# Performance work log

Measured on AMD Instinct MI355X. Metric: run time of the kernel, lower is better.

## Reference

```python
import jax, jax.numpy as jnp
import numpy as np


def _unpack_int4(packed):
    """Unpack bytes (stored as int32 in [0,256)) into signed int4 values in [-8,7].
    packed: [..., K/2] -> [..., K], low nibble first."""
    lo = packed & 0xF
    hi = (packed >> 4) & 0xF
    lo = lo - 16 * (lo >= 8).astype(jnp.int32)
    hi = hi - 16 * (hi >= 8).astype(jnp.int32)
    out = jnp.stack([lo, hi], axis=-1)
    return out.reshape(packed.shape[:-1] + (packed.shape[-1] * 2,))


def setup_inputs() -> dict:
    key = jax.random.key(0)
    ks = jax.random.split(key, 7)
    M, K, N, R = 8192, 4096, 4096, 32
    return {
        "x_quant": jax.random.randint(ks[0], (M, K // 2), 0, 256, dtype=jnp.int32),
        "x_scale": jax.random.uniform(ks[1], (M,), dtype=jnp.float32) * 0.01 + 1e-3,
        "weight": jax.random.randint(ks[2], (N, K // 2), 0, 256, dtype=jnp.int32),
        "weight_scales": jax.random.uniform(ks[3], (N,), dtype=jnp.float32) * 0.01 + 1e-3,
        "bias": jax.random.normal(ks[4], (N,), dtype=jnp.float32) * 0.01,
        "x_r": jax.random.normal(ks[5], (M, R), dtype=jnp.float32),
        "w_outlier": jax.random.normal(ks[6], (N, R), dtype=jnp.float32),
    }


def reference(x_quant, x_scale, weight, weight_scales, bias, x_r, w_outlier):
    # Unpack packed int4 operands: [M,K] and [N,K], values in [-8,7]
    xq = _unpack_int4(x_quant)
    wq = _unpack_int4(weight)
    # Integer GEMM (s4s4 accumulate in int32), then fused dequant + bias
    acc = jnp.matmul(xq, wq.T)  # [M, N] int32
    out = acc.astype(jnp.float32) * x_scale[:, None] * weight_scales[None, :] + bias[None, :]
    # Low-rank outlier correction: addmm_(x_r, w_outlier.T)
    out = out + jnp.matmul(x_r, w_outlier.T)
    return out
```

## Files before the change

kernel.cpp:

```cpp
#include <hip/hip_runtime.h>

#define M_ 8192
#define K_ 4096
#define N_ 4096
#define R_ 32
#define KP_ (K_ / 2)

#define BK 128
#define NKT 32
#define CHUNK 16384
#define GRID ((M_ / 128) * (N_ / 128))

typedef __attribute__((ext_vector_type(4)))  int    i32x4;
typedef __attribute__((ext_vector_type(16))) int    i32x16;
typedef __attribute__((ext_vector_type(4)))  float  f32x4;
typedef __attribute__((ext_vector_type(16))) float  f32x16;
typedef __attribute__((ext_vector_type(8)))  __bf16 bf16x8;

__device__ __forceinline__ void gload16(const void* g, void* l) {
  __builtin_amdgcn_global_load_lds(
      (const __attribute__((address_space(1))) unsigned int*)g,
      (__attribute__((address_space(3))) unsigned int*)l, 16, 0, 0);
}

__device__ __forceinline__ unsigned nib2(int b) {
  unsigned lo = (unsigned)(((b & 15) ^ 8) - 8) & 0xFFu;
  unsigned hi = (unsigned)((((b >> 4) & 15) ^ 8) - 8) & 0xFFu;
  return lo | (hi << 8);
}

__global__ void repack_tiles(const int* __restrict__ in, uint4* __restrict__ out) {
  int i = blockIdx.x * 256 + threadIdx.x;
  int l = i & 63;
  int u = (i >> 6) & 15;
  int tile = i >> 10;
  int row = (tile >> 6) * 256 + (u >> 1) * 32 + (l & 31);
  int w0  = (tile & 63) * 32 + (u & 1) * 16 + (l >> 5) * 8;
  const int4* p = (const int4*)(in + (size_t)row * KP_ + w0);
  int4 a = p[0], b = p[1];
  uint4 o;
  o.x = nib2(a.x) | (nib2(a.y) << 16);
  o.y = nib2(a.z) | (nib2(a.w) << 16);
  o.z = nib2(b.x) | (nib2(b.y) << 16);
  o.w = nib2(b.z) | (nib2(b.w) << 16);
  out[i] = o;
}

__device__ __forceinline__ unsigned short f2b(float x) {
  unsigned u = __float_as_uint(x);
  return (unsigned short)((u + 0x7FFFu + ((u >> 16) & 1u)) >> 16);
}

__global__ void f2bf4(const float* __restrict__ in, unsigned short* __restrict__ out, int n4) {
  int stride = gridDim.x * blockDim.x;
  for (int i = blockIdx.x * blockDim.x + threadIdx.x; i < n4; i += stride) {
    float4 f = ((const float4*)in)[i];
    ushort4 o;
    o.x = f2b(f.x); o.y = f2b(f.y); o.z = f2b(f.z); o.w = f2b(f.w);
    ((ushort4*)out)[i] = o;
  }
}

__global__ __launch_bounds__(256, 3) void gemm_w4a4(
    const char* __restrict__ x8t, const char* __restrict__ w8t,
    const unsigned short* __restrict__ xrb, const unsigned short* __restrict__ wob,
    const float* __restrict__ xscale, const float* __restrict__ wscale,
    const float* __restrict__ bias, float* __restrict__ out)
{
  __shared__ __align__(16) char lds[32768];

  const int t  = threadIdx.x;
  const int w  = t >> 6;
  const int l  = t & 63;
  const int lr = l & 31;
  const int lh = l >> 5;
  const int wr = w >> 1;
  const int wc = w & 1;

  const int xcd = blockIdx.x & 7;
  const int c   = blockIdx.x >> 3;
  const int mt  = (xcd & 3) * 16 + (c & 15);
  const int nt  = (xcd >> 2) * 16 + (c >> 4);
  const int m0  = mt * 128, n0 = nt * 128;

  const char* aT = x8t + (size_t)(mt >> 1) * 64 * CHUNK;
  const char* bT = w8t + (size_t)(nt >> 1) * 64 * CHUNK;
  const int ha = (mt & 1) * 8192;
  const int hb = (nt & 1) * 8192;

  char* ldsA = lds;
  char* ldsB = lds + 16384;

#define STAGE(ktl)                                                            \
  { int q = w >> 1, po = (w & 1) * 4096;                                      \
    const char* sa = aT + (size_t)(2 * (ktl) + q) * CHUNK + ha + po + (l << 4); \
    char* da = ldsA + q * 8192 + po;                                          \
    gload16(sa, da);                gload16(sa + 1024, da + 1024);            \
    gload16(sa + 2048, da + 2048);  gload16(sa + 3072, da + 3072);            \
    const char* sb = bT + (size_t)(2 * (ktl) + q) * CHUNK + hb + po + (l << 4); \
    char* db = ldsB + q * 8192 + po;                                          \
    gload16(sb, db);                gload16(sb + 1024, db + 1024);            \
    gload16(sb + 2048, db + 2048);  gload16(sb + 3072, db + 3072); }

  i32x16 acc[2][2] = {};

  for (int ktl = 0; ktl < NKT; ++ktl) {
    __syncthreads();
    STAGE(ktl)
    __syncthreads();

    #pragma unroll
    for (int ks = 0; ks < 4; ++ks) {
      const int ko = (ks >> 1) * 8192 + (ks & 1) * 1024;
      i32x4 a0 = *(const i32x4*)(ldsA + ko + (wr * 2 + 0) * 2048 + (l << 4));
      i32x4 a1 = *(const i32x4*)(ldsA + ko + (wr * 2 + 1) * 2048 + (l << 4));
      i32x4 b0 = *(const i32x4*)(ldsB + ko + (wc * 2 + 0) * 2048 + (l << 4));
      i32x4 b1 = *(const i32x4*)(ldsB + ko + (wc * 2 + 1) * 2048 + (l << 4));
      acc[0][0] = __builtin_amdgcn_mfma_i32_32x32x32_i8(a0, b0, acc[0][0], 0, 0, 0);
      acc[0][1] = __builtin_amdgcn_mfma_i32_32x32x32_i8(a0, b1, acc[0][1], 0, 0, 0);
      acc[1][0] = __builtin_amdgcn_mfma_i32_32x32x32_i8(a1, b0, acc[1][0], 0, 0, 0);
      acc[1][1] = __builtin_amdgcn_mfma_i32_32x32x32_i8(a1, b1, acc[1][1], 0, 0, 0);
    }
  }

  bf16x8 br0[2], br1[2];
  float swv[2], bv[2];
  #pragma unroll
  for (int ni = 0; ni < 2; ++ni) {
    int cg = n0 + wc * 64 + ni * 32 + lr;
    const unsigned short* pw = wob + (size_t)cg * R_;
    br0[ni] = *(const bf16x8*)(pw + lh * 8);
    br1[ni] = *(const bf16x8*)(pw + 16 + lh * 8);
    swv[ni] = wscale[cg];
    bv[ni]  = bias[cg];
  }

  #pragma unroll
  for (int mi = 0; mi < 2; ++mi) {
    const int rbase = m0 + wr * 64 + mi * 32;
    f32x4 sxg[4];
    #pragma unroll
    for (int g = 0; g < 4; ++g)
      sxg[g] = *(const f32x4*)(xscale + rbase + g * 8 + 4 * lh);
    const unsigned short* px = xrb + (size_t)(rbase + lr) * R_;
    bf16x8 ar0 = *(const bf16x8*)(px + lh * 8);
    bf16x8 ar1 = *(const bf16x8*)(px + 16 + lh * 8);

    #pragma unroll
    for (int ni = 0; ni < 2; ++ni) {
      f32x16 cc = {};
      cc = __builtin_amdgcn_mfma_f32_32x32x16_bf16(ar0, br0[ni], cc, 0, 0, 0);
      cc = __builtin_amdgcn_mfma_f32_32x32x16_bf16(ar1, br1[ni], cc, 0, 0, 0);
      const int cg = n0 + wc * 64 + ni * 32 + lr;
      #pragma unroll
      for (int r = 0; r < 16; ++r) {
        int row = rbase + (r & 3) + 8 * (r >> 2) + 4 * lh;
        out[(size_t)row * N_ + cg] =
            (float)acc[mi][ni][r] * sxg[r >> 2][r & 3] * swv[ni] + cc[r] + bv[ni];
      }
    }
  }
}

extern "C" void kernel_launch(void* const* d_in, const int* in_sizes, int n_in,
                              void* d_out, int out_size, void* d_ws, size_t ws_size,
                              hipStream_t stream) {
  const int*   x_quant   = (const int*)d_in[0];
  const float* x_scale   = (const float*)d_in[1];
  const int*   weight    = (const int*)d_in[2];
  const float* w_scales  = (const float*)d_in[3];
  const float* bias      = (const float*)d_in[4];
  const float* x_r       = (const float*)d_in[5];
  const float* w_outlier = (const float*)d_in[6];
  float* out = (float*)d_out;

  char* ws = (char*)d_ws;
  char*           x8t = ws;
  char*           w8t = ws + (size_t)M_ * K_;
  unsigned short* xrb = (unsigned short*)(ws + (size_t)M_ * K_ + (size_t)N_ * K_);
  unsigned short* wob = xrb + (size_t)M_ * R_;

  repack_tiles<<<(M_ * K_ / 16) / 256, 256, 0, stream>>>(x_quant, (uint4*)x8t);
  repack_tiles<<<(N_ * K_ / 16) / 256, 256, 0, stream>>>(weight,  (uint4*)w8t);
  f2bf4<<<256, 256, 0, stream>>>(x_r, xrb, M_ * R_ / 4);
  f2bf4<<<128, 256, 0, stream>>>(w_outlier, wob, N_ * R_ / 4);

  gemm_w4a4<<<GRID, 256, 0, stream>>>(
      x8t, w8t, xrb, wob, x_scale, w_scales, bias, out);
}
```

Measured before the change: 195.5 us.

## Use 256x256 tiles with 512 threads and triple-buffered async LDS pipeline

Grows the GEMM block tile from 128x128 to 256x256 with 8 waves. K-tiles are staged through a three-deep LDS ring buffer using async global-to-LDS loads issued two iterations ahead, with fine-grained vmcnt waits, raw barriers and s_setprio around the MFMA bursts. The goal is to raise operand reuse per byte loaded and to hide global-load latency behind compute instead of syncing on every tile. In exchange it uses 96KB of LDS and more accumulator registers per thread, which lowers occupancy. It also drops the XCD-aware block swizzle for a simple row-major mapping, which may hurt L2 locality.

```diff
diff --git a/kernel.cpp b/kernel.cpp
--- a/kernel.cpp
+++ b/kernel.cpp
@@ -6,10 +6,10 @@
 #define R_ 32
 #define KP_ (K_ / 2)
 
-#define BK 128
-#define NKT 32
+#define NKT 64
 #define CHUNK 16384
-#define GRID ((M_ / 128) * (N_ / 128))
+#define BUF 32768
+#define GRID ((M_ / 256) * (N_ / 256))
 
 typedef __attribute__((ext_vector_type(4)))  int    i32x4;
 typedef __attribute__((ext_vector_type(16))) int    i32x16;
@@ -61,70 +61,84 @@
   }
 }
 
-__global__ __launch_bounds__(256, 3) void gemm_w4a4(
+__global__ __launch_bounds__(512, 2) void gemm_w4a4(
     const char* __restrict__ x8t, const char* __restrict__ w8t,
     const unsigned short* __restrict__ xrb, const unsigned short* __restrict__ wob,
     const float* __restrict__ xscale, const float* __restrict__ wscale,
     const float* __restrict__ bias, float* __restrict__ out)
 {
-  __shared__ __align__(16) char lds[32768];
+  __shared__ __align__(16) char lds[3 * BUF];
 
   const int t  = threadIdx.x;
   const int w  = t >> 6;
   const int l  = t & 63;
   const int lr = l & 31;
   const int lh = l >> 5;
-  const int wr = w >> 1;
-  const int wc = w & 1;
-
-  const int xcd = blockIdx.x & 7;
-  const int c   = blockIdx.x >> 3;
-  const int mt  = (xcd & 3) * 16 + (c & 15);
-  const int nt  = (xcd >> 2) * 16 + (c >> 4);
-  const int m0  = mt * 128, n0 = nt * 128;
-
-  const char* aT = x8t + (size_t)(mt >> 1) * 64 * CHUNK;
-  const char* bT = w8t + (size_t)(nt >> 1) * 64 * CHUNK;
-  const int ha = (mt & 1) * 8192;
-  const int hb = (nt & 1) * 8192;
-
-  char* ldsA = lds;
-  char* ldsB = lds + 16384;
-
-#define STAGE(ktl)                                                            \
-  { int q = w >> 1, po = (w & 1) * 4096;                                      \
-    const char* sa = aT + (size_t)(2 * (ktl) + q) * CHUNK + ha + po + (l << 4); \
-    char* da = ldsA + q * 8192 + po;                                          \
-    gload16(sa, da);                gload16(sa + 1024, da + 1024);            \
-    gload16(sa + 2048, da + 2048);  gload16(sa + 3072, da + 3072);            \
-    const char* sb = bT + (size_t)(2 * (ktl) + q) * CHUNK + hb + po + (l << 4); \
-    char* db = ldsB + q * 8192 + po;                                          \
-    gload16(sb, db);                gload16(sb + 1024, db + 1024);            \
-    gload16(sb + 2048, db + 2048);  gload16(sb + 3072, db + 3072); }
-
-  i32x16 acc[2][2] = {};
-
-  for (int ktl = 0; ktl < NKT; ++ktl) {
-    __syncthreads();
-    STAGE(ktl)
-    __syncthreads();
-
-    #pragma unroll
-    for (int ks = 0; ks < 4; ++ks) {
-      const int ko = (ks >> 1) * 8192 + (ks & 1) * 1024;
-      i32x4 a0 = *(const i32x4*)(ldsA + ko + (wr * 2 + 0) * 2048 + (l << 4));
-      i32x4 a1 = *(const i32x4*)(ldsA + ko + (wr * 2 + 1) * 2048 + (l << 4));
-      i32x4 b0 = *(const i32x4*)(ldsB + ko + (wc * 2 + 0) * 2048 + (l << 4));
-      i32x4 b1 = *(const i32x4*)(ldsB + ko + (wc * 2 + 1) * 2048 + (l << 4));
-      acc[0][0] = __builtin_amdgcn_mfma_i32_32x32x32_i8(a0, b0, acc[0][0], 0, 0, 0);
-      acc[0][1] = __builtin_amdgcn_mfma_i32_32x32x32_i8(a0, b1, acc[0][1], 0, 0, 0);
-      acc[1][0] = __builtin_amdgcn_mfma_i32_32x32x32_i8(a1, b0, acc[1][0], 0, 0, 0);
-      acc[1][1] = __builtin_amdgcn_mfma_i32_32x32x32_i8(a1, b1, acc[1][1], 0, 0, 0);
-    }
+  const int wr = w >> 2;
+  const int wc = w & 3;
+
+  const int mt = blockIdx.x & 31;
+  const int nt = blockIdx.x >> 5;
+  const int m0 = mt * 256, n0 = nt * 256;
+
+  const char* aT = x8t + (size_t)mt * NKT * CHUNK;
+  const char* bT = w8t + (size_t)nt * NKT * CHUNK;
+
+#define STAGE_A(KT, B_)                                                       \
+  { const char* s = aT + (size_t)(KT) * CHUNK + (t << 4);                     \
+    char* d = lds + (B_) * BUF + (t << 4);                                    \
+    gload16(s, d); gload16(s + 8192, d + 8192); }
+#define STAGE_B(KT, B_)                                                       \
+  { const char* s = bT + (size_t)(KT) * CHUNK + (t << 4);                     \
+    char* d = lds + (B_) * BUF + 16384 + (t << 4);                            \
+    gload16(s, d); gload16(s + 8192, d + 8192); }
+#define FENCE asm volatile("" ::: "memory")
+
+#define PHASE(KS, STAGE_STMT, WAIT_STMT)                                      \
+  { i32x4 af[4], bv[2];                                                       \
+    _Pragma("unroll")                                                         \
+    for (int mi = 0; mi < 4; ++mi)                                            \
+      af[mi] = *(const i32x4*)(Ab + (((wr * 4 + mi) * 2 + (KS)) << 10) + (l << 4)); \
+    _Pragma("unroll")                                                         \
+    for (int nj = 0; nj < 2; ++nj)                                            \
+      bv[nj] = *(const i32x4*)(Bb + (((wc * 2 + nj) * 2 + (KS)) << 10) + (l << 4)); \
+    STAGE_STMT;                                                               \
+    FENCE; __builtin_amdgcn_s_barrier(); FENCE;                               \
+    __builtin_amdgcn_s_setprio(1);                                            \
+    _Pragma("unroll")                                                         \
+    for (int mi = 0; mi < 4; ++mi)                                            \
+      _Pragma("unroll")                                                       \
+      for (int nj = 0; nj < 2; ++nj)                                          \
+        acc[mi][nj] = __builtin_amdgcn_mfma_i32_32x32x32_i8(                  \
+            af[mi], bv[nj], acc[mi][nj], 0, 0, 0);                            \
+    __builtin_amdgcn_s_setprio(0);                                            \
+    WAIT_STMT;                                                                \
+    FENCE; __builtin_amdgcn_s_barrier(); FENCE; }
+
+  i32x16 acc[4][2] = {};
+
+  STAGE_A(0, 0) STAGE_B(0, 0)
+  STAGE_A(1, 1) STAGE_B(1, 1)
+  asm volatile("s_waitcnt vmcnt(4)" ::: "memory");
+  __builtin_amdgcn_s_barrier();
+  FENCE;
+
+  for (int kt = 0; kt < NKT; ++kt) {
+    const char* Ab = lds + (kt % 3) * BUF;
+    const char* Bb = Ab + 16384;
+    const int sb = (kt + 2) % 3;
+
+    PHASE(0,
+          if (kt < NKT - 2) STAGE_A(kt + 2, sb),
+          )
+    PHASE(1,
+          if (kt < NKT - 2) STAGE_B(kt + 2, sb),
+          if (kt < NKT - 2) { asm volatile("s_waitcnt vmcnt(4)" ::: "memory"); }
+          else if (kt == NKT - 2) { asm volatile("s_waitcnt vmcnt(0)" ::: "memory"); })
   }
 
   bf16x8 br0[2], br1[2];
-  float swv[2], bv[2];
+  float swv[2], bv2[2];
   #pragma unroll
   for (int ni = 0; ni < 2; ++ni) {
     int cg = n0 + wc * 64 + ni * 32 + lr;
@@ -132,12 +146,12 @@
     br0[ni] = *(const bf16x8*)(pw + lh * 8);
     br1[ni] = *(const bf16x8*)(pw + 16 + lh * 8);
     swv[ni] = wscale[cg];
-    bv[ni]  = bias[cg];
+    bv2[ni] = bias[cg];
   }
 
   #pragma unroll
-  for (int mi = 0; mi < 2; ++mi) {
-    const int rbase = m0 + wr * 64 + mi * 32;
+  for (int mi = 0; mi < 4; ++mi) {
+    const int rbase = m0 + wr * 128 + mi * 32;
     f32x4 sxg[4];
     #pragma unroll
     for (int g = 0; g < 4; ++g)
@@ -156,7 +170,7 @@
       for (int r = 0; r < 16; ++r) {
         int row = rbase + (r & 3) + 8 * (r >> 2) + 4 * lh;
         out[(size_t)row * N_ + cg] =
-            (float)acc[mi][ni][r] * sxg[r >> 2][r & 3] * swv[ni] + cc[r] + bv[ni];
+            (float)acc[mi][ni][r] * sxg[r >> 2][r & 3] * swv[ni] + cc[r] + bv2[ni];
       }
     }
   }
@@ -185,6 +199,6 @@
   f2bf4<<<256, 256, 0, stream>>>(x_r, xrb, M_ * R_ / 4);
   f2bf4<<<128, 256, 0, stream>>>(w_outlier, wob, N_ * R_ / 4);
 
-  gemm_w4a4<<<GRID, 256, 0, stream>>>(
+  gemm_w4a4<<<GRID, 512, 0, stream>>>(
       x8t, w8t, xrb, wob, x_scale, w_scales, bias, out);
 }
```

Measured after the change: 175.0 us. -10.5%, faster.
